# Kernel tuning notes

Hardware: AMD Instinct MI355X
Metric: run time of the kernel (lower is better)

The kernel has to match this reference:

```python
import jax, jax.numpy as jnp
import numpy as np

ND, NP, NS = 30000, 30000, 10000
HID, NH = 128, 8
HD = HID // NH  # 16
E_DD = E_DP = E_PD = E_PP = 1000000
E_SD = 500000
NEG_SLOPE = 0.2  # DGL GATConv default leaky_relu slope


def _gat(x_src, x_dst, src, dst, W, al, ar, b):
    """Single-relation GATConv (DGL semantics, eval mode / no dropout)."""
    n_dst = x_dst.shape[0]
    z_src = (x_src @ W).reshape(-1, NH, HD)   # [Ns,H,D]
    z_dst = (x_dst @ W).reshape(-1, NH, HD)   # [Nd,H,D]
    el = jnp.sum(z_src * al, axis=-1)          # [Ns,H]
    er = jnp.sum(z_dst * ar, axis=-1)          # [Nd,H]
    e = jax.nn.leaky_relu(el[src] + er[dst], NEG_SLOPE)  # [E,H]
    # edge softmax over incoming edges of each dst node
    emax = jax.ops.segment_max(e, dst, num_segments=n_dst)
    emax = jnp.where(jnp.isfinite(emax), emax, 0.0)
    ex = jnp.exp(e - emax[dst])
    den = jax.ops.segment_sum(ex, dst, num_segments=n_dst)
    attn = ex / jnp.maximum(den[dst], 1e-9)    # [E,H]
    msg = attn[:, :, None] * z_src[src]        # [E,H,D]
    out = jax.ops.segment_sum(msg, dst, num_segments=n_dst)  # [Nd,H,D]
    return out + b.reshape(1, NH, HD)


def _semantic(feats, W1, b1, W2, b2):
    # feats: [N,R,HID]; per-node softmax over relation axis
    s = jnp.tanh(feats @ W1 + b1) @ W2 + b2    # [N,R,1]
    w = jax.nn.softmax(s, axis=1)
    return jnp.sum(feats * w, axis=1)          # [N,HID]


def setup_inputs() -> dict:
    key = jax.random.key(0)
    ks = jax.random.split(key, 40)
    it = iter(range(40))
    def nrm(shape, scale=1.0):
        return jax.random.normal(ks[next(it)], shape, dtype=jnp.float32) * scale
    sc = 1.0 / float(np.sqrt(HID))
    inp = {}
    inp["h_drug"] = nrm((ND, HID))
    inp["h_protein"] = nrm((NP, HID))
    inp["h_se"] = nrm((NS, HID))
    for rel in ["dd", "dp", "pd", "pp", "sd"]:
        inp[f"W_{rel}"] = nrm((HID, HID), sc)
        inp[f"al_{rel}"] = nrm((NH, HD), sc)
        inp[f"ar_{rel}"] = nrm((NH, HD), sc)
        inp[f"b_{rel}"] = jnp.zeros((HID,), dtype=jnp.float32)
    inp["W1"] = nrm((HID, HID), sc)
    inp["b1"] = jnp.zeros((HID,), dtype=jnp.float32)
    inp["W2"] = nrm((HID, 1), sc)
    inp["b2"] = jnp.zeros((1,), dtype=jnp.float32)
    def ridx(n, e):
        return jax.random.randint(ks[next(it)], (e,), 0, n, dtype=jnp.int32)
    inp["src_dd"] = ridx(ND, E_DD); inp["dst_dd"] = ridx(ND, E_DD)
    inp["src_dp"] = ridx(ND, E_DP); inp["dst_dp"] = ridx(NP, E_DP)
    inp["src_pd"] = ridx(NP, E_PD); inp["dst_pd"] = ridx(ND, E_PD)
    inp["src_pp"] = ridx(NP, E_PP); inp["dst_pp"] = ridx(NP, E_PP)
    inp["src_sd"] = ridx(NS, E_SD); inp["dst_sd"] = ridx(ND, E_SD)
    return inp


def reference(h_drug, h_protein, h_se,
              W_dd, al_dd, ar_dd, b_dd, W_dp, al_dp, ar_dp, b_dp,
              W_pd, al_pd, ar_pd, b_pd, W_pp, al_pp, ar_pp, b_pp,
              W_sd, al_sd, ar_sd, b_sd, W1, b1, W2, b2,
              src_dd, dst_dd, src_dp, dst_dp, src_pd, dst_pd,
              src_pp, dst_pp, src_sd, dst_sd):
    # per-relation GAT message passing (HeteroGraphConv, aggregate='stack')
    o_dd = _gat(h_drug, h_drug, src_dd, dst_dd, W_dd, al_dd, ar_dd, b_dd)
    o_pd = _gat(h_protein, h_drug, src_pd, dst_pd, W_pd, al_pd, ar_pd, b_pd)
    o_sd = _gat(h_se, h_drug, src_sd, dst_sd, W_sd, al_sd, ar_sd, b_sd)
    o_dp = _gat(h_drug, h_protein, src_dp, dst_dp, W_dp, al_dp, ar_dp, b_dp)
    o_pp = _gat(h_protein, h_protein, src_pp, dst_pp, W_pp, al_pp, ar_pp, b_pp)
    drug_stack = jnp.stack([o_dd, o_pd, o_sd], axis=1).reshape(ND, 3, HID)
    prot_stack = jnp.stack([o_dp, o_pp], axis=1).reshape(NP, 2, HID)
    out_drug = _semantic(drug_stack, W1, b1, W2, b2)
    out_protein = _semantic(prot_stack, W1, b1, W2, b2)
    return out_drug, out_protein
```

## Files before the change

### kernel.cpp

```cpp
#include <hip/hip_runtime.h>
#include <hip/hip_bf16.h>

typedef unsigned short u16;
typedef __attribute__((ext_vector_type(8))) short short8;
typedef __attribute__((ext_vector_type(4))) float f32x4;

#define ND 30000
#define NP 30000
#define NS 10000
#define CSTRIDE 30016
#define ETOT 4500000
#define CHUNK 9216
#define NC 489
#define NBR 118
#define NB 590

__device__ __forceinline__ float bf2f(u16 u) {
  union { unsigned int i; float f; } c; c.i = ((unsigned int)u) << 16; return c.f;
}
__device__ __forceinline__ u16 f2bf(float f) {
  union { float f; unsigned int i; } c; c.f = f;
  unsigned int u = c.i;
  unsigned int r = (u + 0x7fffu + ((u >> 16) & 1u)) >> 16;
  return (u16)r;
}

__device__ __forceinline__ int detect_isbf(const void* x) {
  __shared__ int cnt4[4];
  const int tid = threadIdx.x;
  const u16 v = ((const u16*)x)[2 * tid];
  const int e = (v >> 7) & 0xff;
  const unsigned long long m = __ballot(e >= 100 && e <= 140);
  if ((tid & 63) == 0) cnt4[tid >> 6] = __popcll(m);
  __syncthreads();
  const int sane = cnt4[0] + cnt4[1] + cnt4[2] + cnt4[3];
  return sane >= 200;
}

__device__ __forceinline__ float ld_in(const void* p, int i, int isbf) {
  return isbf ? bf2f(((const u16*)p)[i]) : ((const float*)p)[i];
}

struct EJobs { const int* src[5]; const int* dst[5]; };
__device__ __forceinline__ int e_job(int e) {
  return (e >= 1000000) + (e >= 2000000) + (e >= 2500000) + (e >= 3500000);
}
__device__ __forceinline__ int e_base(int j) {
  const int base[6] = {0, 1000000, 2000000, 2500000, 3500000, 4500000};
  return base[j];
}

struct PJobs { const void* W[5]; const void* al[5]; const void* ar[5];
               float* wal[5]; float* war[5]; };
__device__ void prep_dev(const PJobs& J, int b, int isbf) {
  const int tid = threadIdx.x;
  if (tid >= 128) return;
  const int k = tid;
  for (int h = 0; h < 8; ++h) {
    float sa = 0.f, sr = 0.f;
    for (int d = 0; d < 16; ++d) {
      const float wv = ld_in(J.W[b], k * 128 + h * 16 + d, isbf);
      sa = fmaf(wv, ld_in(J.al[b], h * 16 + d, isbf), sa);
      sr = fmaf(wv, ld_in(J.ar[b], h * 16 + d, isbf), sr);
    }
    J.wal[b][h * 128 + k] = sa;
    J.war[b][h * 128 + k] = sr;
  }
}

__device__ void hist_dev(const EJobs& J, int* __restrict__ ghist, int c) {
  __shared__ int hsh[NB];
  const int tid = threadIdx.x;
  for (int i = tid; i < NB; i += 256) hsh[i] = 0;
  __syncthreads();
  const int e0 = c * CHUNK;
  #pragma unroll 4
  for (int t = 0; t < 36; ++t) {
    const int e = e0 + t * 256 + tid;
    if (e < ETOT) {
      const int j = e_job(e);
      const int d = J.dst[j][e - e_base(j)];
      atomicAdd(&hsh[j * NBR + (d >> 8)], 1);
    }
  }
  __syncthreads();
  for (int i = tid; i < NB; i += 256) ghist[c * NB + i] = hsh[i];
}

__global__ __launch_bounds__(256) void k_front(PJobs PJ, EJobs EJ,
    const void* xdet, int* __restrict__ ghist) {
  if (blockIdx.x < 5) {
    const int isbf = detect_isbf(xdet);
    prep_dev(PJ, blockIdx.x, isbf);
  } else {
    hist_dev(EJ, ghist, blockIdx.x - 5);
  }
}

struct KPack { const void* W[6]; const float* wal[6]; const float* war[6];
               u16* out[6]; };
__device__ void pack_dev(const KPack& J, int b, int isbf) {
  const int job = b / 9;
  const int i0 = (b % 9) * 2048 + threadIdx.x * 8;
  const int kc = i0 / 4608;
  const int rem = i0 - kc * 4608;
  const int n = rem >> 5;
  const int q = (rem >> 3) & 3;
  u16 vals[8];
  #pragma unroll
  for (int j = 0; j < 8; ++j) {
    const int k = kc * 32 + q * 8 + j;
    float v;
    if (job == 5)      v = (n < 128) ? ld_in(J.W[5], k * 128 + n, isbf) : 0.f;
    else if (n < 128)  v = ld_in(J.W[job], k * 128 + n, isbf);
    else if (n < 136)  v = J.wal[job][(n - 128) * 128 + k];
    else               v = J.war[job][(n - 136) * 128 + k];
    vals[j] = f2bf(v);
  }
  *(uint4*)&J.out[job][i0] = *(uint4*)vals;
}

__device__ void bucketscan_dev(const int* __restrict__ ghist,
    int* __restrict__ gcur, int* __restrict__ totals, int b) {
  __shared__ int ts[256];
  const int tid = threadIdx.x;
  int v0 = 0, v1 = 0;
  const int c0 = tid * 2;
  if (c0 < NC) v0 = ghist[c0 * NB + b];
  if (c0 + 1 < NC) v1 = ghist[(c0 + 1) * NB + b];
  ts[tid] = v0 + v1;
  __syncthreads();
  for (int o = 1; o < 256; o <<= 1) {
    const int x = (tid >= o) ? ts[tid - o] : 0;
    __syncthreads();
    ts[tid] += x;
    __syncthreads();
  }
  int run = (tid == 0) ? 0 : ts[tid - 1];
  if (c0 < NC) { gcur[b * NC + c0] = run; run += v0; }
  if (c0 + 1 < NC) gcur[b * NC + c0 + 1] = run;
  if (tid == 255) totals[b] = ts[255];
}

__global__ __launch_bounds__(256) void k_mid(KPack KJ, const void* xdet,
    const int* __restrict__ ghist, int* __restrict__ gcur, int* __restrict__ totals) {
  if (blockIdx.x < 54) {
    const int isbf = detect_isbf(xdet);
    pack_dev(KJ, blockIdx.x, isbf);
  } else {
    bucketscan_dev(ghist, gcur, totals, blockIdx.x - 54);
  }
}

__device__ void base_from_totals(const int* __restrict__ totals, int* bsh) {
  __shared__ int ts[256];
  const int tid = threadIdx.x;
  const int i0 = tid * 3;
  int v0 = 0, v1 = 0, v2 = 0;
  if (i0 < NB) v0 = totals[i0];
  if (i0 + 1 < NB) v1 = totals[i0 + 1];
  if (i0 + 2 < NB) v2 = totals[i0 + 2];
  ts[tid] = v0 + v1 + v2;
  __syncthreads();
  for (int o = 1; o < 256; o <<= 1) {
    const int x = (tid >= o) ? ts[tid - o] : 0;
    __syncthreads();
    ts[tid] += x;
    __syncthreads();
  }
  int run = (tid == 0) ? 0 : ts[tid - 1];
  if (i0 < NB) { bsh[i0] = run; run += v0; }
  if (i0 + 1 < NB) { bsh[i0 + 1] = run; run += v1; }
  if (i0 + 2 < NB) bsh[i0 + 2] = run;
  if (tid == 0) bsh[NB] = ETOT;
  __syncthreads();
}

__global__ __launch_bounds__(256) void k_bin(EJobs J,
    const int* __restrict__ gcur, const int* __restrict__ totals,
    unsigned int* __restrict__ bin) {
  __shared__ int bsh[NB + 1];
  __shared__ int cur[NB];
  base_from_totals(totals, bsh);
  const int c = blockIdx.x, tid = threadIdx.x;
  for (int i = tid; i < NB; i += 256) cur[i] = bsh[i] + gcur[i * NC + c];
  __syncthreads();
  const int e0 = c * CHUNK;
  #pragma unroll 4
  for (int t = 0; t < 36; ++t) {
    const int e = e0 + t * 256 + tid;
    if (e < ETOT) {
      const int j = e_job(e);
      const int le = e - e_base(j);
      const int d = J.dst[j][le];
      const int s = J.src[j][le];
      const int pos = atomicAdd(&cur[j * NBR + (d >> 8)], 1);
      bin[pos] = ((unsigned int)(d & 255) << 16) | (unsigned int)s;
    }
  }
}

__device__ void fill2_dev(const unsigned int* __restrict__ bin,
    const int* __restrict__ totals, u16* __restrict__ csr,
    int* __restrict__ offsets, int b) {
  __shared__ int bsh2[NB + 1];
  __shared__ int cnt[256], curs[256];
  base_from_totals(totals, bsh2);
  const int tid = threadIdx.x;
  const int rel = b / NBR;
  const int bloc = b - rel * NBR;
  const int d0 = bloc << 8;
  const int gbeg = bsh2[b];
  const int n = bsh2[b + 1] - gbeg;
  cnt[tid] = 0;
  __syncthreads();
  for (int i = tid; i < n; i += 256)
    atomicAdd(&cnt[bin[gbeg + i] >> 16], 1);
  __syncthreads();
  const int orig = cnt[tid];
  for (int o = 1; o < 256; o <<= 1) {
    const int x = (tid >= o) ? cnt[tid - o] : 0;
    __syncthreads();
    cnt[tid] += x;
    __syncthreads();
  }
  const int ex = cnt[tid] - orig;
  curs[tid] = ex;
  const int ebr = e_base(rel);
  const int d = d0 + tid;
  if (d < 30000) offsets[rel * CSTRIDE + d] = (gbeg - ebr) + ex;
  if (bloc == NBR - 1 && tid == 0)
    offsets[rel * CSTRIDE + 30000] = e_base(rel + 1) - ebr;
  __syncthreads();
  for (int i = tid; i < n; i += 256) {
    const unsigned int v = bin[gbeg + i];
    const int pos = atomicAdd(&curs[v >> 16], 1);
    csr[gbeg + pos] = (u16)(v & 0xffffu);
  }
}

struct XJobs {
  const void* x[8]; const u16* bp[8]; u16* z[8]; float* el[8]; float* er[8];
  int N[8]; int t0[8]; int blk0[9];
};
__device__ void xform_dev(const XJobs& J, int xb, int isbf) {
  __shared__ __align__(16) u16 Bf[18432];
  __shared__ __align__(16) u16 As[64 * 136];
  const int tid = threadIdx.x;
  int job = 0;
  while (xb >= J.blk0[job + 1]) ++job;
  const int row0 = (xb - J.blk0[job]) * 64;
  const int N = J.N[job];
  const int t0 = J.t0[job];
  const u16* bp = J.bp[job];
  const void* x = J.x[job];

  if (t0 == 0) {
    for (int i = tid * 8; i < 18432; i += 2048)
      *(uint4*)&Bf[i] = *(const uint4*)&bp[i];
  } else {
    const int i = tid * 8;
    const int kc = i >> 9;
    const int off = (kc * 144 + 128) * 32 + (i & 511);
    *(uint4*)&Bf[off] = *(const uint4*)&bp[off];
  }

  if (isbf) {
    const uint4* xv = (const uint4*)x;
    for (int i = tid; i < 1024; i += 256) {
      const int r = i >> 4, c8 = i & 15;
      const int row = row0 + r;
      uint4 v = make_uint4(0, 0, 0, 0);
      if (row < N) v = xv[row * 16 + c8];
      *(uint4*)&As[r * 136 + c8 * 8] = v;
    }
  } else {
    const float4* xf = (const float4*)x;
    for (int i = tid; i < 2048; i += 256) {
      const int r = i >> 5, c4 = i & 31;
      const int row = row0 + r;
      unsigned long long pkv = 0ull;
      if (row < N) {
        const float4 v = xf[row * 32 + c4];
        pkv = (unsigned long long)f2bf(v.x) | ((unsigned long long)f2bf(v.y) << 16)
            | ((unsigned long long)f2bf(v.z) << 32) | ((unsigned long long)f2bf(v.w) << 48);
      }
      *(unsigned long long*)&As[r * 136 + c4 * 4] = pkv;
    }
  }
  __syncthreads();

  const int wave = tid >> 6;
  const int lane = tid & 63;
  const int q = lane >> 4;
  const int c = lane & 15;

  f32x4 accT[8];
  f32x4 acc8 = (f32x4){0.f, 0.f, 0.f, 0.f};
  if (t0 == 0) {
    #pragma unroll
    for (int t = 0; t < 8; ++t) accT[t] = (f32x4){0.f, 0.f, 0.f, 0.f};
  }

  #pragma unroll
  for (int kc = 0; kc < 4; ++kc) {
    const short8 a = *(const short8*)&As[(wave * 16 + c) * 136 + kc * 32 + q * 8];
    if (t0 == 0) {
      #pragma unroll
      for (int t = 0; t < 8; ++t) {
        const short8 bb = *(const short8*)&Bf[((kc * 144 + t * 16 + c) * 4 + q) * 8];
        accT[t] = __builtin_amdgcn_mfma_f32_16x16x32_bf16(a, bb, accT[t], 0, 0, 0);
      }
    }
    const short8 b8 = *(const short8*)&Bf[((kc * 144 + 128 + c) * 4 + q) * 8];
    acc8 = __builtin_amdgcn_mfma_f32_16x16x32_bf16(a, b8, acc8, 0, 0, 0);
  }

  const int rbase = row0 + wave * 16 + q * 4;
  if (t0 == 0 && J.z[job]) {
    u16* zo = J.z[job];
    #pragma unroll
    for (int t = 0; t < 8; ++t)
      #pragma unroll
      for (int r = 0; r < 4; ++r) {
        const int row = rbase + r;
        if (row < N) zo[row * 128 + t * 16 + c] = f2bf(accT[t][r]);
      }
  }
  #pragma unroll
  for (int r = 0; r < 4; ++r) {
    const int row = rbase + r;
    if (row < N) {
      const float v = acc8[r];
      if (c < 8) { if (J.el[job]) J.el[job][row * 8 + c] = v; }
      else       { if (J.er[job]) J.er[job][row * 8 + (c - 8)] = v; }
    }
  }
}

__global__ __launch_bounds__(256) void k_l4(XJobs XJ, const void* xdet,
    const unsigned int* __restrict__ bin, const int* __restrict__ totals,
    u16* __restrict__ csr, int* __restrict__ offsets) {
  if (blockIdx.x < NB) {
    fill2_dev(bin, totals, csr, offsets, blockIdx.x);
  } else {
    const int isbf = detect_isbf(xdet);
    xform_dev(XJ, blockIdx.x - NB, isbf);
  }
}

struct AJobs { const u16* csr[5]; const int* off[5]; const float* el[5];
               const float* er[5]; const u16* z[5]; const void* b[5];
               u16* feats[5]; int stride[5]; };
__global__ __launch_bounds__(256) void k_agg_all(AJobs J, const void* xdet) {
  const int isbf = detect_isbf(xdet);
  const int gw = (blockIdx.x * 256 + threadIdx.x) >> 6;
  const int lane = threadIdx.x & 63;
  const int job = gw / 30000;
  const int d = gw - job * 30000;
  const int h = lane >> 3;
  const int i8 = lane & 7;
  const float* el = J.el[job];
  const u16* ztl = J.z[job] + lane * 2;
  const u16* csr = J.csr[job];
  const float erh = J.er[job][d * 8 + h];
  const int beg = J.off[job][d];
  const int end = J.off[job][d + 1];
  const int gb4 = (lane & 56) << 2;

  float a0 = 0.f, a1 = 0.f, denP = 0.f;
  for (int p = beg; p < end; p += 8) {
    const int idx = p + i8;
    const bool valid = (idx < end);
    const int sE = (int)csr[valid ? idx : (end - 1)];
    float eh = el[sE * 8 + h] + erh;
    eh = fminf(fmaxf(eh, 0.2f * eh), 60.f);
    const float exE = valid ? __expf(eh) : 0.f;
    denP += exE;
    int si[8];
    #pragma unroll
    for (int i = 0; i < 8; ++i) si[i] = __builtin_amdgcn_readlane(sE, i);
    unsigned int zp[8];
    #pragma unroll
    for (int i = 0; i < 8; ++i)
      zp[i] = *(const unsigned int*)(ztl + si[i] * 128);
    const int exb = __float_as_int(exE);
    float exi[8];
    #pragma unroll
    for (int i = 0; i < 8; ++i)
      exi[i] = __int_as_float(__builtin_amdgcn_ds_bpermute(gb4 + i * 4, exb));
    #pragma unroll
    for (int i = 0; i < 8; ++i) {
      union { unsigned int u; float f; } lo, hi;
      lo.u = zp[i] << 16; hi.u = zp[i] & 0xffff0000u;
      a0 = fmaf(exi[i], lo.f, a0);
      a1 = fmaf(exi[i], hi.f, a1);
    }
  }
  denP += __shfl_xor(denP, 1);
  denP += __shfl_xor(denP, 2);
  denP += __shfl_xor(denP, 4);
  const float inv = 1.f / fmaxf(denP, 1e-9f);
  const int j0 = lane * 2;
  const float v0 = a0 * inv + ld_in(J.b[job], j0, isbf);
  const float v1 = a1 * inv + ld_in(J.b[job], j0 + 1, isbf);
  const unsigned int packed = (unsigned int)f2bf(v0) | ((unsigned int)f2bf(v1) << 16);
  *(unsigned int*)(J.feats[job] + d * J.stride[job] + j0) = packed;
}

__global__ __launch_bounds__(256) void k_sem_all(
    const u16* __restrict__ f, const u16* __restrict__ w1pack,
    const void* __restrict__ b1, const void* __restrict__ W2,
    const void* __restrict__ b2, float* __restrict__ s_out, int total,
    const void* xdet)
{
  __shared__ __align__(16) u16 Bf[18432];
  __shared__ __align__(16) u16 As[64 * 136];
  __shared__ float b1S[128], W2S[128];
  const int isbf = detect_isbf(xdet);
  const int tid = threadIdx.x;
  const int row0 = blockIdx.x * 64;

  for (int i = tid * 8; i < 18432; i += 2048)
    *(uint4*)&Bf[i] = *(const uint4*)&w1pack[i];
  if (tid < 128) { b1S[tid] = ld_in(b1, tid, isbf); W2S[tid] = ld_in(W2, tid, isbf); }
  {
    const uint4* xv = (const uint4*)f;
    for (int i = tid; i < 1024; i += 256) {
      const int r = i >> 4, c8 = i & 15;
      const int row = row0 + r;
      uint4 v = make_uint4(0, 0, 0, 0);
      if (row < total) v = xv[row * 16 + c8];
      *(uint4*)&As[r * 136 + c8 * 8] = v;
    }
  }
  __syncthreads();

  const int wave = tid >> 6;
  const int lane = tid & 63;
  const int q = lane >> 4;
  const int c = lane & 15;

  f32x4 acc[8];
  #pragma unroll
  for (int t = 0; t < 8; ++t) acc[t] = (f32x4){0.f, 0.f, 0.f, 0.f};

  #pragma unroll
  for (int kc = 0; kc < 4; ++kc) {
    const short8 a = *(const short8*)&As[(wave * 16 + c) * 136 + kc * 32 + q * 8];
    #pragma unroll
    for (int t = 0; t < 8; ++t) {
      const short8 bb = *(const short8*)&Bf[((kc * 144 + t * 16 + c) * 4 + q) * 8];
      acc[t] = __builtin_amdgcn_mfma_f32_16x16x32_bf16(a, bb, acc[t], 0, 0, 0);
    }
  }

  float part[4] = {0.f, 0.f, 0.f, 0.f};
  #pragma unroll
  for (int t = 0; t < 8; ++t) {
    const int n = t * 16 + c;
    const float b1v = b1S[n];
    const float w2v = W2S[n];
    #pragma unroll
    for (int r = 0; r < 4; ++r) {
      const float hv = acc[t][r] + b1v;
      const float e = __expf(2.f * hv);
      const float th = 1.f - 2.f / (e + 1.f);
      part[r] = fmaf(th, w2v, part[r]);
    }
  }
  #pragma unroll
  for (int r = 0; r < 4; ++r) {
    part[r] += __shfl_xor(part[r], 1);
    part[r] += __shfl_xor(part[r], 2);
    part[r] += __shfl_xor(part[r], 4);
    part[r] += __shfl_xor(part[r], 8);
  }
  if (c == 0) {
    const float b2v = ld_in(b2, 0, isbf);
    #pragma unroll
    for (int r = 0; r < 4; ++r) {
      const int row = row0 + wave * 16 + q * 4 + r;
      if (row < total) s_out[row] = part[r] + b2v;
    }
  }
}

__global__ __launch_bounds__(256) void k_combine_all(
    const u16* __restrict__ feats, const float* __restrict__ s,
    void* __restrict__ out, const void* xdet)
{
  const int isbf = detect_isbf(xdet);
  const int i = blockIdx.x * 256 + threadIdx.x;
  if (i >= 3840000) return;
  const bool drug = (i < 1920000);
  const int li = drug ? i : i - 1920000;
  const int n = li >> 6;
  const int j2 = li & 63;
  const float* sr = s + (drug ? n * 3 : 90000 + n * 2);
  const u16* fb = feats + (drug ? n * 384 : 11520000 + n * 256) + j2 * 2;
  const float s0v = sr[0];
  const float s1v = sr[1];
  const float s2v = drug ? sr[2] : -3.4e38f;
  const float m = fmaxf(fmaxf(s0v, s1v), s2v);
  const float w0 = __expf(s0v - m);
  const float w1 = __expf(s1v - m);
  const float w2 = drug ? __expf(s2v - m) : 0.f;
  const float inv = 1.f / (w0 + w1 + w2);
  const unsigned int f0 = *(const unsigned int*)(fb);
  const unsigned int f1 = *(const unsigned int*)(fb + 128);
  union { unsigned int u; float f; } t;
  float acc0, acc1;
  t.u = f0 << 16;          acc0 = w0 * t.f;
  t.u = f0 & 0xffff0000u;  acc1 = w0 * t.f;
  t.u = f1 << 16;          acc0 = fmaf(w1, t.f, acc0);
  t.u = f1 & 0xffff0000u;  acc1 = fmaf(w1, t.f, acc1);
  if (drug) {
    const unsigned int f2 = *(const unsigned int*)(fb + 256);
    t.u = f2 << 16;          acc0 = fmaf(w2, t.f, acc0);
    t.u = f2 & 0xffff0000u;  acc1 = fmaf(w2, t.f, acc1);
  }
  acc0 *= inv; acc1 *= inv;
  const int oidx = drug ? i : i;
  if (isbf) {
    const unsigned int packed = (unsigned int)f2bf(acc0) | ((unsigned int)f2bf(acc1) << 16);
    ((unsigned int*)out)[oidx] = packed;
  } else {
    float2 v; v.x = acc0; v.y = acc1;
    ((float2*)out)[oidx] = v;
  }
}

extern "C" void kernel_launch(void* const* d_in, const int* in_sizes, int n_in,
                              void* d_out, int out_size, void* d_ws, size_t ws_size,
                              hipStream_t stream)
{
  (void)in_sizes; (void)n_in; (void)out_size; (void)ws_size;

  const void* h_drug = d_in[0];
  const void* h_prot = d_in[1];
  const void* h_se   = d_in[2];
  const void* W_dd = d_in[3];  const void* al_dd = d_in[4];
  const void* ar_dd = d_in[5]; const void* b_dd  = d_in[6];
  const void* W_dp = d_in[7];  const void* al_dp = d_in[8];
  const void* ar_dp = d_in[9]; const void* b_dp  = d_in[10];
  const void* W_pd = d_in[11]; const void* al_pd = d_in[12];
  const void* ar_pd = d_in[13];const void* b_pd  = d_in[14];
  const void* W_pp = d_in[15]; const void* al_pp = d_in[16];
  const void* ar_pp = d_in[17];const void* b_pp  = d_in[18];
  const void* W_sd = d_in[19]; const void* al_sd = d_in[20];
  const void* ar_sd = d_in[21];const void* b_sd  = d_in[22];
  const void* W1 = d_in[23];   const void* b1 = d_in[24];
  const void* W2 = d_in[25];   const void* b2 = d_in[26];
  const int* src_dd = (const int*)d_in[27];
  const int* dst_dd = (const int*)d_in[28];
  const int* src_dp = (const int*)d_in[29];
  const int* dst_dp = (const int*)d_in[30];
  const int* src_pd = (const int*)d_in[31];
  const int* dst_pd = (const int*)d_in[32];
  const int* src_pp = (const int*)d_in[33];
  const int* dst_pp = (const int*)d_in[34];
  const int* src_sd = (const int*)d_in[35];
  const int* dst_sd = (const int*)d_in[36];

  char* w = (char*)d_ws;
  float* el5   = (float*)(w);
  float* er5   = (float*)(w + 4800000);
  u16* z_dd    = (u16*)(w + 9600000);
  u16* z_pd    = (u16*)(w + 17280000);
  u16* z_sd    = (u16*)(w + 24960000);
  u16* z_dp    = (u16*)(w + 27520000);
  u16* z_pp    = (u16*)(w + 35200000);
  int* offsets = (int*)(w + 42880000);
  u16* csr     = (u16*)(w + 43480320);
  int* ghist   = (int*)(w + 52480320);
  int* gcur    = (int*)(w + 53634560);
  int* totals  = (int*)(w + 54788608);
  float* s     = (float*)(w + 54791168);
  u16* feats   = (u16*)(w + 55391232);
  unsigned int* bin = (unsigned int*)(w + 55391232);
  float* ww    = (float*)(w + 93791232);
  u16* packs   = (u16*)(w + 93832192);

  float *wal[5], *war[5];
  for (int r = 0; r < 5; ++r) { wal[r] = ww + r * 2048; war[r] = ww + r * 2048 + 1024; }
  u16* pk[6];
  for (int r = 0; r < 6; ++r) pk[r] = packs + r * 18432;
  float* el_r[5]; float* er_r[5];
  for (int r = 0; r < 5; ++r) { el_r[r] = el5 + r * 240000; er_r[r] = er5 + r * 240000; }
  u16* feats_d = feats;
  u16* feats_p = feats + 11520000;

  const dim3 blk(256);

  PJobs pj;
  pj.W[0]=W_dd; pj.al[0]=al_dd; pj.ar[0]=ar_dd;
  pj.W[1]=W_pd; pj.al[1]=al_pd; pj.ar[1]=ar_pd;
  pj.W[2]=W_sd; pj.al[2]=al_sd; pj.ar[2]=ar_sd;
  pj.W[3]=W_dp; pj.al[3]=al_dp; pj.ar[3]=ar_dp;
  pj.W[4]=W_pp; pj.al[4]=al_pp; pj.ar[4]=ar_pp;
  for (int r = 0; r < 5; ++r) { pj.wal[r] = wal[r]; pj.war[r] = war[r]; }

  EJobs ej;
  ej.src[0]=src_dd; ej.dst[0]=dst_dd;
  ej.src[1]=src_pd; ej.dst[1]=dst_pd;
  ej.src[2]=src_sd; ej.dst[2]=dst_sd;
  ej.src[3]=src_dp; ej.dst[3]=dst_dp;
  ej.src[4]=src_pp; ej.dst[4]=dst_pp;

  KPack kp;
  kp.W[0]=W_dd; kp.W[1]=W_pd; kp.W[2]=W_sd; kp.W[3]=W_dp; kp.W[4]=W_pp; kp.W[5]=W1;
  for (int r = 0; r < 5; ++r) { kp.wal[r] = wal[r]; kp.war[r] = war[r]; }
  kp.wal[5]=nullptr; kp.war[5]=nullptr;
  for (int r = 0; r < 6; ++r) kp.out[r] = pk[r];

  XJobs xj;
  auto setx = [&](int i, const void* x, const u16* bp, u16* z, float* el,
                  float* er, int N, int t0) {
    xj.x[i]=x; xj.bp[i]=bp; xj.z[i]=z; xj.el[i]=el; xj.er[i]=er; xj.N[i]=N; xj.t0[i]=t0;
  };
  setx(0, h_drug, pk[0], z_dd, el_r[0], er_r[0], ND, 0);
  setx(1, h_prot, pk[1], z_pd, el_r[1], nullptr, NP, 0);
  setx(2, h_drug, pk[1], nullptr, nullptr, er_r[1], ND, 8);
  setx(3, h_se,   pk[2], z_sd, el_r[2], nullptr, NS, 0);
  setx(4, h_drug, pk[2], nullptr, nullptr, er_r[2], ND, 8);
  setx(5, h_drug, pk[3], z_dp, el_r[3], nullptr, ND, 0);
  setx(6, h_prot, pk[3], nullptr, nullptr, er_r[3], NP, 8);
  setx(7, h_prot, pk[4], z_pp, el_r[4], er_r[4], NP, 0);
  int xblocks = 0;
  for (int i = 0; i < 8; ++i) { xj.blk0[i] = xblocks; xblocks += (xj.N[i] + 63) / 64; }
  xj.blk0[8] = xblocks;

  AJobs aj;
  const int ebase[5] = {0, 1000000, 2000000, 2500000, 3500000};
  const void* bias[5] = {b_dd, b_pd, b_sd, b_dp, b_pp};
  u16* fb[5] = {feats_d, feats_d + 128, feats_d + 256, feats_p, feats_p + 128};
  const int fstride[5] = {384, 384, 384, 256, 256};
  const u16* zz[5] = {z_dd, z_pd, z_sd, z_dp, z_pp};
  for (int r = 0; r < 5; ++r) {
    aj.csr[r] = csr + ebase[r];
    aj.off[r] = offsets + r * CSTRIDE;
    aj.el[r] = el_r[r];
    aj.er[r] = er_r[r];
    aj.z[r] = zz[r];
    aj.b[r] = bias[r];
    aj.feats[r] = fb[r];
    aj.stride[r] = fstride[r];
  }

  k_front<<<dim3(5 + NC), blk, 0, stream>>>(pj, ej, h_drug, ghist);
  k_mid<<<dim3(54 + NB), blk, 0, stream>>>(kp, h_drug, ghist, gcur, totals);
  k_bin<<<dim3(NC), blk, 0, stream>>>(ej, gcur, totals, bin);
  k_l4<<<dim3(NB + xblocks), blk, 0, stream>>>(xj, h_drug, bin, totals, csr, offsets);
  k_agg_all<<<dim3(37500), blk, 0, stream>>>(aj, h_drug);
  k_sem_all<<<dim3((150000 + 63) / 64), blk, 0, stream>>>(feats, pk[5], b1, W2, b2, s, 150000, h_drug);
  k_combine_all<<<dim3(15000), blk, 0, stream>>>(feats, s, d_out, h_drug);
}
```

Measured before the change: 543.0 us.

## Split z into head-halves and run aggregation in two passes per destination

The projection kernel now writes z as two head-half planes (64 columns each) instead of interleaved 128-wide rows. The aggregation kernel runs two passes per destination node, one per half, each with twice as many waves. Each wave handles 16 edges per iteration, split across its two 32-lane halves, and combines the halves with shuffles at the end. The aim is a smaller gather footprint per pass for better cache locality and more parallelism. The cost is re-reading the CSR and el values twice and extra bpermute and shuffle work.

```diff
diff --git a/kernel.cpp b/kernel.cpp
--- a/kernel.cpp
+++ b/kernel.cpp
@@ -320,12 +320,14 @@
   if (t0 == 0 && J.z[job]) {
     u16* zo = J.z[job];
     #pragma unroll
-    for (int t = 0; t < 8; ++t)
+    for (int t = 0; t < 8; ++t) {
+      u16* zh = zo + (t >> 2) * N * 64;
       #pragma unroll
       for (int r = 0; r < 4; ++r) {
         const int row = rbase + r;
-        if (row < N) zo[row * 128 + t * 16 + c] = f2bf(accT[t][r]);
+        if (row < N) zh[row * 64 + (t & 3) * 16 + c] = f2bf(accT[t][r]);
       }
+    }
   }
   #pragma unroll
   for (int r = 0; r < 4; ++r) {
@@ -351,61 +353,71 @@
 
 struct AJobs { const u16* csr[5]; const int* off[5]; const float* el[5];
                const float* er[5]; const u16* z[5]; const void* b[5];
-               u16* feats[5]; int stride[5]; };
+               u16* feats[5]; int stride[5]; int nsrc[5]; };
 __global__ __launch_bounds__(256) void k_agg_all(AJobs J, const void* xdet) {
   const int isbf = detect_isbf(xdet);
   const int gw = (blockIdx.x * 256 + threadIdx.x) >> 6;
   const int lane = threadIdx.x & 63;
-  const int job = gw / 30000;
-  const int d = gw - job * 30000;
-  const int h = lane >> 3;
-  const int i8 = lane & 7;
+  const int pass = (gw >= 150000) ? 1 : 0;
+  const int rw = gw - pass * 150000;
+  const int job = rw / 30000;
+  const int d = rw - job * 30000;
+  const int dim2 = lane & 31;
+  const int hx = (lane >> 3) & 3;
+  const int eidx = ((lane & 32) >> 2) + (lane & 7);
   const float* el = J.el[job];
-  const u16* ztl = J.z[job] + lane * 2;
+  const u16* zh = J.z[job] + pass * J.nsrc[job] * 64;
   const u16* csr = J.csr[job];
-  const float erh = J.er[job][d * 8 + h];
+  const float erh = J.er[job][d * 8 + pass * 4 + hx];
   const int beg = J.off[job][d];
   const int end = J.off[job][d + 1];
-  const int gb4 = (lane & 56) << 2;
+  const int exbase = ((lane & 32) << 2) + hx * 32;
+  const int srcbase = lane & 32;
 
   float a0 = 0.f, a1 = 0.f, denP = 0.f;
-  for (int p = beg; p < end; p += 8) {
-    const int idx = p + i8;
-    const bool valid = (idx < end);
-    const int sE = (int)csr[valid ? idx : (end - 1)];
-    float eh = el[sE * 8 + h] + erh;
+  for (int p = beg; p < end; p += 16) {
+    const int ci = p + (lane & 15);
+    const int sE = (int)csr[ci < end ? ci : end - 1];
+    const int sx = __builtin_amdgcn_ds_bpermute(4 * eidx, sE);
+    float eh = el[sx * 8 + pass * 4 + hx] + erh;
     eh = fminf(fmaxf(eh, 0.2f * eh), 60.f);
-    const float exE = valid ? __expf(eh) : 0.f;
+    const float exE = (p + eidx < end) ? __expf(eh) : 0.f;
     denP += exE;
-    int si[8];
-    #pragma unroll
-    for (int i = 0; i < 8; ++i) si[i] = __builtin_amdgcn_readlane(sE, i);
+    const int exb = __float_as_int(exE);
+    int sj[8];
+    #pragma unroll
+    for (int j = 0; j < 8; ++j)
+      sj[j] = __builtin_amdgcn_ds_bpermute(srcbase + 4 * j, sE);
     unsigned int zp[8];
     #pragma unroll
-    for (int i = 0; i < 8; ++i)
-      zp[i] = *(const unsigned int*)(ztl + si[i] * 128);
-    const int exb = __float_as_int(exE);
+    for (int j = 0; j < 8; ++j)
+      zp[j] = *(const unsigned int*)(zh + sj[j] * 64 + dim2 * 2);
     float exi[8];
     #pragma unroll
-    for (int i = 0; i < 8; ++i)
-      exi[i] = __int_as_float(__builtin_amdgcn_ds_bpermute(gb4 + i * 4, exb));
-    #pragma unroll
-    for (int i = 0; i < 8; ++i) {
+    for (int j = 0; j < 8; ++j)
+      exi[j] = __int_as_float(__builtin_amdgcn_ds_bpermute(exbase + 4 * j, exb));
+    #pragma unroll
+    for (int j = 0; j < 8; ++j) {
       union { unsigned int u; float f; } lo, hi;
-      lo.u = zp[i] << 16; hi.u = zp[i] & 0xffff0000u;
-      a0 = fmaf(exi[i], lo.f, a0);
-      a1 = fmaf(exi[i], hi.f, a1);
+      lo.u = zp[j] << 16; hi.u = zp[j] & 0xffff0000u;
+      a0 = fmaf(exi[j], lo.f, a0);
+      a1 = fmaf(exi[j], hi.f, a1);
     }
   }
   denP += __shfl_xor(denP, 1);
   denP += __shfl_xor(denP, 2);
   denP += __shfl_xor(denP, 4);
-  const float inv = 1.f / fmaxf(denP, 1e-9f);
-  const int j0 = lane * 2;
-  const float v0 = a0 * inv + ld_in(J.b[job], j0, isbf);
-  const float v1 = a1 * inv + ld_in(J.b[job], j0 + 1, isbf);
-  const unsigned int packed = (unsigned int)f2bf(v0) | ((unsigned int)f2bf(v1) << 16);
-  *(unsigned int*)(J.feats[job] + d * J.stride[job] + j0) = packed;
+  denP += __shfl_xor(denP, 32);
+  a0 += __shfl_xor(a0, 32);
+  a1 += __shfl_xor(a1, 32);
+  if (lane < 32) {
+    const float inv = 1.f / fmaxf(denP, 1e-9f);
+    const int j0 = pass * 64 + dim2 * 2;
+    const float v0 = a0 * inv + ld_in(J.b[job], j0, isbf);
+    const float v1 = a1 * inv + ld_in(J.b[job], j0 + 1, isbf);
+    const unsigned int packed = (unsigned int)f2bf(v0) | ((unsigned int)f2bf(v1) << 16);
+    *(unsigned int*)(J.feats[job] + d * J.stride[job] + j0) = packed;
+  }
 }
 
 __global__ __launch_bounds__(256) void k_sem_all(
@@ -521,13 +533,12 @@
     t.u = f2 & 0xffff0000u;  acc1 = fmaf(w2, t.f, acc1);
   }
   acc0 *= inv; acc1 *= inv;
-  const int oidx = drug ? i : i;
   if (isbf) {
     const unsigned int packed = (unsigned int)f2bf(acc0) | ((unsigned int)f2bf(acc1) << 16);
-    ((unsigned int*)out)[oidx] = packed;
+    ((unsigned int*)out)[i] = packed;
   } else {
     float2 v; v.x = acc0; v.y = acc1;
-    ((float2*)out)[oidx] = v;
+    ((float2*)out)[i] = v;
   }
 }
 
@@ -636,6 +647,7 @@
   const void* bias[5] = {b_dd, b_pd, b_sd, b_dp, b_pp};
   u16* fb[5] = {feats_d, feats_d + 128, feats_d + 256, feats_p, feats_p + 128};
   const int fstride[5] = {384, 384, 384, 256, 256};
+  const int nsrc5[5] = {ND, NP, NS, ND, NP};
   const u16* zz[5] = {z_dd, z_pd, z_sd, z_dp, z_pp};
   for (int r = 0; r < 5; ++r) {
     aj.csr[r] = csr + ebase[r];
@@ -646,13 +658,14 @@
     aj.b[r] = bias[r];
     aj.feats[r] = fb[r];
     aj.stride[r] = fstride[r];
+    aj.nsrc[r] = nsrc5[r];
   }
 
   k_front<<<dim3(5 + NC), blk, 0, stream>>>(pj, ej, h_drug, ghist);
   k_mid<<<dim3(54 + NB), blk, 0, stream>>>(kp, h_drug, ghist, gcur, totals);
   k_bin<<<dim3(NC), blk, 0, stream>>>(ej, gcur, totals, bin);
   k_l4<<<dim3(NB + xblocks), blk, 0, stream>>>(xj, h_drug, bin, totals, csr, offsets);
-  k_agg_all<<<dim3(37500), blk, 0, stream>>>(aj, h_drug);
+  k_agg_all<<<dim3(75000), blk, 0, stream>>>(aj, h_drug);
   k_sem_all<<<dim3((150000 + 63) / 64), blk, 0, stream>>>(feats, pk[5], b1, W2, b2, s, 150000, h_drug);
   k_combine_all<<<dim3(15000), blk, 0, stream>>>(feats, s, d_out, h_drug);
 }
```

Result: slower. 615.1 us (+13.3%).

## Fuse semantic scoring and relation-softmax combine into one kernel

Applied to the files above, without the earlier changes.

Merges the semantic-attention scoring kernel and the combine kernel into a single kernel. Each block now loads whole nodes' relation rows (63 rows for drugs, 64 for proteins), computes scores, does the per-node softmax in shared memory, and writes the weighted output straight from LDS. This removes one launch, the global score array, and the second read of the feature stack. In exchange there are more blocks, drug blocks leave one row idle, and the b2 bias is dropped because it cancels in the softmax.

```diff
diff --git a/kernel.cpp b/kernel.cpp
--- a/kernel.cpp
+++ b/kernel.cpp
@@ -14,6 +14,8 @@
 #define NC 489
 #define NBR 118
 #define NB 590
+#define NBD 1429
+#define NBP 938
 
 __device__ __forceinline__ float bf2f(u16 u) {
   union { unsigned int i; float f; } c; c.i = ((unsigned int)u) << 16; return c.f;
@@ -408,18 +410,22 @@
   *(unsigned int*)(J.feats[job] + d * J.stride[job] + j0) = packed;
 }
 
-__global__ __launch_bounds__(256) void k_sem_all(
+__global__ __launch_bounds__(256) void k_semco(
     const u16* __restrict__ f, const u16* __restrict__ w1pack,
     const void* __restrict__ b1, const void* __restrict__ W2,
-    const void* __restrict__ b2, float* __restrict__ s_out, int total,
-    const void* xdet)
+    void* __restrict__ out, const void* xdet)
 {
   __shared__ __align__(16) u16 Bf[18432];
   __shared__ __align__(16) u16 As[64 * 136];
   __shared__ float b1S[128], W2S[128];
+  __shared__ float sS[64];
+  __shared__ float wS[128];
   const int isbf = detect_isbf(xdet);
   const int tid = threadIdx.x;
-  const int row0 = blockIdx.x * 64;
+  const bool drug = (blockIdx.x < NBD);
+  const int bloc = drug ? blockIdx.x : blockIdx.x - NBD;
+  const int row0 = drug ? bloc * 63 : 90000 + bloc * 64;
+  const int rowLim = drug ? 90000 : 150000;
 
   for (int i = tid * 8; i < 18432; i += 2048)
     *(uint4*)&Bf[i] = *(const uint4*)&w1pack[i];
@@ -430,7 +436,7 @@
       const int r = i >> 4, c8 = i & 15;
       const int row = row0 + r;
       uint4 v = make_uint4(0, 0, 0, 0);
-      if (row < total) v = xv[row * 16 + c8];
+      if (row < rowLim) v = xv[row * 16 + c8];
       *(uint4*)&As[r * 136 + c8 * 8] = v;
     }
   }
@@ -477,57 +483,59 @@
     part[r] += __shfl_xor(part[r], 8);
   }
   if (c == 0) {
-    const float b2v = ld_in(b2, 0, isbf);
-    #pragma unroll
-    for (int r = 0; r < 4; ++r) {
-      const int row = row0 + wave * 16 + q * 4 + r;
-      if (row < total) s_out[row] = part[r] + b2v;
-    }
-  }
-}
-
-__global__ __launch_bounds__(256) void k_combine_all(
-    const u16* __restrict__ feats, const float* __restrict__ s,
-    void* __restrict__ out, const void* xdet)
-{
-  const int isbf = detect_isbf(xdet);
-  const int i = blockIdx.x * 256 + threadIdx.x;
-  if (i >= 3840000) return;
-  const bool drug = (i < 1920000);
-  const int li = drug ? i : i - 1920000;
-  const int n = li >> 6;
-  const int j2 = li & 63;
-  const float* sr = s + (drug ? n * 3 : 90000 + n * 2);
-  const u16* fb = feats + (drug ? n * 384 : 11520000 + n * 256) + j2 * 2;
-  const float s0v = sr[0];
-  const float s1v = sr[1];
-  const float s2v = drug ? sr[2] : -3.4e38f;
-  const float m = fmaxf(fmaxf(s0v, s1v), s2v);
-  const float w0 = __expf(s0v - m);
-  const float w1 = __expf(s1v - m);
-  const float w2 = drug ? __expf(s2v - m) : 0.f;
-  const float inv = 1.f / (w0 + w1 + w2);
-  const unsigned int f0 = *(const unsigned int*)(fb);
-  const unsigned int f1 = *(const unsigned int*)(fb + 128);
-  union { unsigned int u; float f; } t;
-  float acc0, acc1;
-  t.u = f0 << 16;          acc0 = w0 * t.f;
-  t.u = f0 & 0xffff0000u;  acc1 = w0 * t.f;
-  t.u = f1 << 16;          acc0 = fmaf(w1, t.f, acc0);
-  t.u = f1 & 0xffff0000u;  acc1 = fmaf(w1, t.f, acc1);
-  if (drug) {
-    const unsigned int f2 = *(const unsigned int*)(fb + 256);
-    t.u = f2 << 16;          acc0 = fmaf(w2, t.f, acc0);
-    t.u = f2 & 0xffff0000u;  acc1 = fmaf(w2, t.f, acc1);
-  }
-  acc0 *= inv; acc1 *= inv;
-  const int oidx = drug ? i : i;
-  if (isbf) {
-    const unsigned int packed = (unsigned int)f2bf(acc0) | ((unsigned int)f2bf(acc1) << 16);
-    ((unsigned int*)out)[oidx] = packed;
-  } else {
-    float2 v; v.x = acc0; v.y = acc1;
-    ((float2*)out)[oidx] = v;
+    #pragma unroll
+    for (int r = 0; r < 4; ++r)
+      sS[wave * 16 + q * 4 + r] = part[r];
+  }
+  __syncthreads();
+
+  const int R = drug ? 3 : 2;
+  const int nmax = drug ? 21 : 32;
+  int nnode = 30000 - bloc * nmax;
+  if (nnode > nmax) nnode = nmax;
+  if (tid < nnode) {
+    const float s0v = sS[tid * R];
+    const float s1v = sS[tid * R + 1];
+    const float s2v = (R == 3) ? sS[tid * R + 2] : -3.4e38f;
+    const float mx = fmaxf(fmaxf(s0v, s1v), s2v);
+    const float w0 = __expf(s0v - mx);
+    const float w1 = __expf(s1v - mx);
+    const float w2 = (R == 3) ? __expf(s2v - mx) : 0.f;
+    const float inv = 1.f / (w0 + w1 + w2);
+    wS[tid * 4 + 0] = w0 * inv;
+    wS[tid * 4 + 1] = w1 * inv;
+    wS[tid * 4 + 2] = w2 * inv;
+  }
+  __syncthreads();
+
+  const int node0 = bloc * nmax;
+  const int tot = nnode * 64;
+  for (int idx = tid; idx < tot; idx += 256) {
+    const int node = idx >> 6;
+    const int j2 = idx & 63;
+    const int lr = node * R;
+    const float w0 = wS[node * 4], w1 = wS[node * 4 + 1], w2 = wS[node * 4 + 2];
+    const unsigned int f0 = *(const unsigned int*)&As[lr * 136 + j2 * 2];
+    const unsigned int f1 = *(const unsigned int*)&As[(lr + 1) * 136 + j2 * 2];
+    union { unsigned int u; float ff; } t;
+    float acc0, acc1;
+    t.u = f0 << 16;          acc0 = w0 * t.ff;
+    t.u = f0 & 0xffff0000u;  acc1 = w0 * t.ff;
+    t.u = f1 << 16;          acc0 = fmaf(w1, t.ff, acc0);
+    t.u = f1 & 0xffff0000u;  acc1 = fmaf(w1, t.ff, acc1);
+    if (drug) {
+      const unsigned int f2v = *(const unsigned int*)&As[(lr + 2) * 136 + j2 * 2];
+      t.u = f2v << 16;         acc0 = fmaf(w2, t.ff, acc0);
+      t.u = f2v & 0xffff0000u; acc1 = fmaf(w2, t.ff, acc1);
+    }
+    const int oi = (drug ? 0 : 1920000) + (node0 + node) * 64 + j2;
+    if (isbf) {
+      ((unsigned int*)out)[oi] =
+          (unsigned int)f2bf(acc0) | ((unsigned int)f2bf(acc1) << 16);
+    } else {
+      float2 v; v.x = acc0; v.y = acc1;
+      ((float2*)out)[oi] = v;
+    }
   }
 }
 
@@ -552,6 +560,7 @@
   const void* ar_sd = d_in[21];const void* b_sd  = d_in[22];
   const void* W1 = d_in[23];   const void* b1 = d_in[24];
   const void* W2 = d_in[25];   const void* b2 = d_in[26];
+  (void)b2;
   const int* src_dd = (const int*)d_in[27];
   const int* dst_dd = (const int*)d_in[28];
   const int* src_dp = (const int*)d_in[29];
@@ -576,7 +585,6 @@
   int* ghist   = (int*)(w + 52480320);
   int* gcur    = (int*)(w + 53634560);
   int* totals  = (int*)(w + 54788608);
-  float* s     = (float*)(w + 54791168);
   u16* feats   = (u16*)(w + 55391232);
   unsigned int* bin = (unsigned int*)(w + 55391232);
   float* ww    = (float*)(w + 93791232);
@@ -653,6 +661,5 @@
   k_bin<<<dim3(NC), blk, 0, stream>>>(ej, gcur, totals, bin);
   k_l4<<<dim3(NB + xblocks), blk, 0, stream>>>(xj, h_drug, bin, totals, csr, offsets);
   k_agg_all<<<dim3(37500), blk, 0, stream>>>(aj, h_drug);
-  k_sem_all<<<dim3((150000 + 63) / 64), blk, 0, stream>>>(feats, pk[5], b1, W2, b2, s, 150000, h_drug);
-  k_combine_all<<<dim3(15000), blk, 0, stream>>>(feats, s, d_out, h_drug);
-}
+  k_semco<<<dim3(NBD + NBP), blk, 0, stream>>>(feats, pk[5], b1, W2, d_out, h_drug);
+}
```

After: 534.2 us. No clear change (-1.6%).
